# Optimization experiments

Hardware: AMD Instinct MI355X
Metric: run time of the kernel (lower is better)

## Reference

```python
import jax, jax.numpy as jnp
import numpy as np

B, T, DE, DD, A, FN, FS = 32, 2000, 512, 1024, 128, 32, 16
TEMPERATURE = 1.0


def setup_inputs() -> dict:
    key = jax.random.key(0)
    ks = jax.random.split(key, 10)
    input_enc = jax.random.normal(ks[0], (B, T, DE), dtype=jnp.float32)
    # lengths in [T//2, T] so no zero-length utterances
    enc_lengths = jax.random.randint(ks[1], (B,), T // 2, T + 1, dtype=jnp.int32)
    input_dec = jax.random.normal(ks[2], (B, DD), dtype=jnp.float32)
    # prev_att: previous-step attention weights (masked, normalized)
    prev_att = jax.random.uniform(ks[3], (B, T), dtype=jnp.float32)
    pad = jnp.arange(T)[None, :] >= enc_lengths[:, None]
    prev_att = jnp.where(pad, 0.0, prev_att)
    prev_att = prev_att / jnp.sum(prev_att, axis=1, keepdims=True)
    # parameters
    conv_w = jax.random.normal(ks[4], (FN, 1, 2 * FS + 1), dtype=jnp.float32) * 0.1  # [out,in,k]
    enc_w = jax.random.normal(ks[5], (A, DE), dtype=jnp.float32) * 0.04
    dec_w = jax.random.normal(ks[6], (A, DD), dtype=jnp.float32) * 0.03
    att_w = jax.random.normal(ks[7], (A, FN), dtype=jnp.float32) * 0.17
    att_b = jnp.zeros((A,), dtype=jnp.float32)
    out_w = jax.random.normal(ks[8], (1, A), dtype=jnp.float32) * 0.09
    return dict(input_enc=input_enc, enc_lengths=enc_lengths, input_dec=input_dec,
                prev_att=prev_att, conv_w=conv_w, enc_w=enc_w, dec_w=dec_w,
                att_w=att_w, att_b=att_b, out_w=out_w)


def reference(input_enc, enc_lengths, input_dec, prev_att,
              conv_w, enc_w, dec_w, att_w, att_b, out_w):
    b, t, _ = input_enc.shape
    fs = (conv_w.shape[-1] - 1) // 2  # 'same' padding
    # padding mask: True at padded positions t >= length
    mask = jnp.arange(t)[None, :] >= enc_lengths[:, None]  # [B,T]
    # location features: Conv1d over prev attention, 1 -> FN channels, same length
    conv = jax.lax.conv_general_dilated(
        prev_att[:, None, :], conv_w, window_strides=(1,),
        padding=[(fs, fs)], dimension_numbers=("NCH", "OIH", "NCH"))  # [B,FN,T]
    loc_feat = conv.transpose(0, 2, 1)  # [B,T,FN]
    projected_att = loc_feat @ att_w.T + att_b        # [B,T,A]
    projected_enc = input_enc @ enc_w.T               # [B,T,A]
    projected_dec = (input_dec @ dec_w.T)[:, None, :]  # [B,1,A]
    score = jnp.squeeze(jnp.tanh(projected_att + projected_enc + projected_dec) @ out_w.T, -1)  # [B,T]
    score = jnp.where(mask, -jnp.inf, score)
    att_weight = jax.nn.softmax(TEMPERATURE * score, axis=1)  # [B,T]
    context = jnp.einsum("btd,bt->bd", input_enc, att_weight)  # [B,DE]
    return context, att_weight
```

## Files before the change

### kernel.cpp

```cpp
#include <hip/hip_runtime.h>
#include <hip/hip_bf16.h>
#include <math.h>

#define B_ 32
#define T_ 2000
#define DE_ 512
#define DD_ 1024
#define A_ 128
#define FN_ 32
#define FS_ 16
#define KW_ (2*FS_+1)

typedef __bf16 bf16x8 __attribute__((ext_vector_type(8)));
typedef __bf16 bf16x4 __attribute__((ext_vector_type(4)));
typedef float f32x4 __attribute__((ext_vector_type(4)));

#define BT 64

__device__ __forceinline__ void load_lds16(const void* g, void* l) {
    __builtin_amdgcn_global_load_lds(
        (const __attribute__((address_space(1))) unsigned int*)g,
        (__attribute__((address_space(3))) unsigned int*)l, 16, 0, 0);
}

__global__ __launch_bounds__(256) void prep_kernel(
    const float* __restrict__ enc_w, const float* __restrict__ att_w,
    const float* __restrict__ input_dec, const float* __restrict__ dec_w,
    const float* __restrict__ att_b,
    __bf16* __restrict__ enc_bf, __bf16* __restrict__ att_bf,
    float* __restrict__ pdec, float* __restrict__ ctx_un )
{
    int bx = blockIdx.x, tid = threadIdx.x;
    if (bx < 64) {
        int i = bx * 256 + tid;
        float4 v = ((const float4*)enc_w)[i];
        bf16x4 o;
        o[0] = (__bf16)v.x; o[1] = (__bf16)v.y; o[2] = (__bf16)v.z; o[3] = (__bf16)v.w;
        *(bf16x4*)(enc_bf + (size_t)i * 4) = o;
        if (i < (A_ * FN_) / 4) {
            float4 w = ((const float4*)att_w)[i];
            bf16x4 p;
            p[0] = (__bf16)w.x; p[1] = (__bf16)w.y; p[2] = (__bf16)w.z; p[3] = (__bf16)w.w;
            *(bf16x4*)(att_bf + (size_t)i * 4) = p;
        }
    } else if (bx < 192) {
        int pb = bx - 64;
        int b  = pb >> 2;
        int a0 = (pb & 3) * 32;
        int al = tid >> 3;
        int kg = tid & 7;
        int a  = a0 + al;
        const float4* w = (const float4*)(dec_w + (size_t)a * DD_);
        const float4* x = (const float4*)(input_dec + (size_t)b * DD_);
        float acc = 0.f;
        #pragma unroll 8
        for (int j = 0; j < 32; j++) {
            int i4 = kg + j * 8;
            float4 wv = w[i4], xv = x[i4];
            acc += wv.x * xv.x + wv.y * xv.y + wv.z * xv.z + wv.w * xv.w;
        }
        acc += __shfl_xor(acc, 1, 64);
        acc += __shfl_xor(acc, 2, 64);
        acc += __shfl_xor(acc, 4, 64);
        if (kg == 0) pdec[b * A_ + a] = acc + att_b[a];
    } else {
        int idx = (bx - 192) * 256 + tid;
        if (idx < (B_ * DE_ + B_) / 4 + 1)
            ((float4*)ctx_un)[idx] = make_float4(0.f, 0.f, 0.f, 0.f);
    }
}

__global__ __launch_bounds__(256, 4) void score_kernel(
    const float* __restrict__ input_enc, const __bf16* __restrict__ enc_bf,
    const float* __restrict__ prev_att,  const float* __restrict__ conv_w,
    const __bf16* __restrict__ att_bf,   const float* __restrict__ pdec,
    const float* __restrict__ out_w,     const int* __restrict__ lengths,
    float* __restrict__ wbuf, float* __restrict__ ctx_un,
    float* __restrict__ denom)
{
    __shared__ __align__(16) char Bt[16384];
    __shared__ __align__(16) float cw_s[KW_ * FN_];
    __shared__ float pa_s[BT + 2 * FS_];
    __shared__ __align__(16) float w_s[BT];

    const int tid = threadIdx.x;
    const int b  = blockIdx.y;
    const int t0 = blockIdx.x * BT;
    const int len = lengths[b];

    if (t0 >= len) {
        int t = t0 + tid;
        if (tid < BT && t < T_) wbuf[b * T_ + t] = 0.f;
        return;
    }

    const int lane = tid & 63;
    const int wv   = tid >> 6;
    const int col  = lane & 15;
    const int grp  = lane >> 4;
    const int rowb = wv * 16 + col;
    const int t_row = t0 + rowb;
    const int t_clamp = t_row < T_ ? t_row : T_ - 1;
    const float* arow = input_enc + ((size_t)(b * T_ + t_clamp)) * DE_ + grp * 8;

    #pragma unroll
    for (int j = 0; j < 2; j++) {
        int s  = j * 256 + tid;
        int r  = s >> 2;
        int c  = (s & 3) ^ (r & 3);
        load_lds16(enc_bf + (size_t)r * DE_ + c * 8,
                   Bt + j * 4096 + wv * 1024);
    }
    float4 p0 = *(const float4*)(arow);
    float4 p1 = *(const float4*)(arow + 4);

    for (int j = tid; j < BT + 2 * FS_; j += 256) {
        int t = t0 - FS_ + j;
        pa_s[j] = (t >= 0 && t < T_) ? prev_att[b * T_ + t] : 0.f;
    }
    for (int idx = tid; idx < FN_ * KW_; idx += 256) {
        int f = idx / KW_, k = idx % KW_;
        cw_s[k * FN_ + f] = conv_w[idx];
    }
    __syncthreads();

    float cf[8] = {0.f,0.f,0.f,0.f,0.f,0.f,0.f,0.f};
    #pragma unroll
    for (int k = 0; k < KW_; k++) {
        float pa = pa_s[rowb + k];
        float4 c0 = *(const float4*)(cw_s + k * FN_ + grp * 8);
        float4 c1 = *(const float4*)(cw_s + k * FN_ + grp * 8 + 4);
        cf[0] += pa * c0.x; cf[1] += pa * c0.y; cf[2] += pa * c0.z; cf[3] += pa * c0.w;
        cf[4] += pa * c1.x; cf[5] += pa * c1.y; cf[6] += pa * c1.z; cf[7] += pa * c1.w;
    }

    f32x4 acc[8];
    const f32x4 zero = (f32x4){0.f, 0.f, 0.f, 0.f};

    {
        bf16x8 afrag;
        #pragma unroll
        for (int j = 0; j < 8; j++) afrag[j] = (__bf16)cf[j];
        #pragma unroll
        for (int i = 0; i < 8; i++) {
            bf16x8 bfrag = *(const bf16x8*)(att_bf + (size_t)(i * 16 + col) * FN_ + grp * 8);
            acc[i] = __builtin_amdgcn_mfma_f32_16x16x32_bf16(afrag, bfrag, zero, 0, 0, 0);
        }
    }

    const int dsoff = (grp ^ (col & 3)) * 16;

    #pragma unroll
    for (int k = 0; k < 16; k++) {
        __syncthreads();
        float4 n0, n1;
        if (k < 15) {
            int kc_next = (k + 1) * 32;
            char* half = Bt + (((k + 1) & 1) << 13);
            #pragma unroll
            for (int j = 0; j < 2; j++) {
                int s  = j * 256 + tid;
                int r  = s >> 2;
                int c  = (s & 3) ^ (r & 3);
                load_lds16(enc_bf + (size_t)r * DE_ + kc_next + c * 8,
                           half + j * 4096 + wv * 1024);
            }
            n0 = *(const float4*)(arow + kc_next);
            n1 = *(const float4*)(arow + kc_next + 4);
        }
        bf16x8 af;
        af[0] = (__bf16)p0.x; af[1] = (__bf16)p0.y;
        af[2] = (__bf16)p0.z; af[3] = (__bf16)p0.w;
        af[4] = (__bf16)p1.x; af[5] = (__bf16)p1.y;
        af[6] = (__bf16)p1.z; af[7] = (__bf16)p1.w;
        const char* half = Bt + ((k & 1) << 13);
        #pragma unroll
        for (int i = 0; i < 8; i++) {
            bf16x8 bfrag = *(const bf16x8*)(half + (i * 16 + col) * 64 + dsoff);
            acc[i] = __builtin_amdgcn_mfma_f32_16x16x32_bf16(af, bfrag, acc[i], 0, 0, 0);
        }
        p0 = n0; p1 = n1;
    }

    float s[4] = {0.f, 0.f, 0.f, 0.f};
    float Mabs = 0.f;
    #pragma unroll
    for (int i = 0; i < 8; i++) {
        int a = i * 16 + col;
        float ow = out_w[a];
        Mabs += fabsf(ow);
        float bias = pdec[b * A_ + a];
        #pragma unroll
        for (int r = 0; r < 4; r++) {
            float v = acc[i][r] + bias;
            v = fminf(fmaxf(v, -15.f), 15.f);
            float e = __expf(2.f * v);
            s[r] += ow * ((e - 1.f) / (e + 1.f));
        }
    }
    #pragma unroll
    for (int r = 0; r < 4; r++) {
        s[r] += __shfl_xor(s[r], 1, 64);
        s[r] += __shfl_xor(s[r], 2, 64);
        s[r] += __shfl_xor(s[r], 4, 64);
        s[r] += __shfl_xor(s[r], 8, 64);
    }
    Mabs += __shfl_xor(Mabs, 1, 64);
    Mabs += __shfl_xor(Mabs, 2, 64);
    Mabs += __shfl_xor(Mabs, 4, 64);
    Mabs += __shfl_xor(Mabs, 8, 64);

    if (col == 0) {
        int tb = wv * 16 + grp * 4;
        float4 wvec;
        float* wp = &wvec.x;
        #pragma unroll
        for (int r = 0; r < 4; r++) {
            int t = t0 + tb + r;
            wp[r] = (t < len) ? __expf(s[r] - Mabs) : 0.f;
        }
        *(float4*)(w_s + tb) = wvec;
        if (t0 + tb < T_) *(float4*)(wbuf + b * T_ + t0 + tb) = wvec;
    }
    __syncthreads();

    if (tid < 64) {
        float w = w_s[tid];
        w += __shfl_xor(w, 1, 64);
        w += __shfl_xor(w, 2, 64);
        w += __shfl_xor(w, 4, 64);
        w += __shfl_xor(w, 8, 64);
        w += __shfl_xor(w, 16, 64);
        w += __shfl_xor(w, 32, 64);
        if (tid == 0) atomicAdd(&denom[b], w);
    }

    int n_eff = len - t0;
    if (n_eff > BT) n_eff = BT;
    {
        int tg = tid >> 7;
        int d0 = (tid & 127) * 4;
        const float* ebase = input_enc + ((size_t)(b * T_ + t0)) * DE_ + d0;
        float cx = 0.f, cy = 0.f, cz = 0.f, cw = 0.f;
        #pragma unroll 4
        for (int t = tg; t < n_eff; t += 2) {
            float w = w_s[t];
            float4 v = *(const float4*)(ebase + (size_t)t * DE_);
            cx += w * v.x; cy += w * v.y; cz += w * v.z; cw += w * v.w;
        }
        atomicAdd(&ctx_un[b * DE_ + d0 + 0], cx);
        atomicAdd(&ctx_un[b * DE_ + d0 + 1], cy);
        atomicAdd(&ctx_un[b * DE_ + d0 + 2], cz);
        atomicAdd(&ctx_un[b * DE_ + d0 + 3], cw);
    }
}

__global__ __launch_bounds__(256) void finalize_kernel(
    const float* __restrict__ wbuf, const float* __restrict__ ctx_un,
    const float* __restrict__ denom, float* __restrict__ out)
{
    int bx = blockIdx.x, tid = threadIdx.x;
    if (bx < 64) {
        int i4 = bx * 256 + tid;
        if (i4 < (B_ * T_) / 4) {
            int b = i4 / (T_ / 4);
            float inv = 1.f / denom[b];
            float4 w = ((const float4*)wbuf)[i4];
            w.x *= inv; w.y *= inv; w.z *= inv; w.w *= inv;
            ((float4*)(out + B_ * DE_))[i4] = w;
        }
    } else {
        int j = (bx - 64) * 256 + tid;
        int b = j / (DE_ / 4);
        float inv = 1.f / denom[b];
        float4 c = ((const float4*)ctx_un)[j];
        c.x *= inv; c.y *= inv; c.z *= inv; c.w *= inv;
        ((float4*)out)[j] = c;
    }
}

extern "C" void kernel_launch(void* const* d_in, const int* in_sizes, int n_in,
                              void* d_out, int out_size, void* d_ws, size_t ws_size,
                              hipStream_t stream)
{
    const float* input_enc   = (const float*)d_in[0];
    const int*   enc_lengths = (const int*)d_in[1];
    const float* input_dec   = (const float*)d_in[2];
    const float* prev_att    = (const float*)d_in[3];
    const float* conv_w      = (const float*)d_in[4];
    const float* enc_w       = (const float*)d_in[5];
    const float* dec_w       = (const float*)d_in[6];
    const float* att_w       = (const float*)d_in[7];
    const float* att_b       = (const float*)d_in[8];
    const float* out_w       = (const float*)d_in[9];

    float* out = (float*)d_out;
    char* ws = (char*)d_ws;
    float*  pdec   = (float*)ws;
    float*  wbuf   = (float*)(ws + 16384);
    __bf16* enc_bf = (__bf16*)(ws + 272384);
    __bf16* att_bf = (__bf16*)(ws + 403456);
    float*  ctx_un = (float*)(ws + 411648);
    float*  denom  = (float*)(ws + 477184);

    prep_kernel<<<209, 256, 0, stream>>>(enc_w, att_w, input_dec, dec_w, att_b,
                                         enc_bf, att_bf, pdec, ctx_un);

    dim3 sgrid((T_ + BT - 1) / BT, B_);
    score_kernel<<<sgrid, 256, 0, stream>>>(input_enc, enc_bf, prev_att, conv_w,
                                            att_bf, pdec, out_w, enc_lengths,
                                            wbuf, ctx_un, denom);

    finalize_kernel<<<80, 256, 0, stream>>>(wbuf, ctx_un, denom, out);
}
```

Baseline: 227.3 us.

## Double score kernel time tile to 128 rows with two accumulator sets per wave

```diff
diff --git a/kernel.cpp b/kernel.cpp
--- a/kernel.cpp
+++ b/kernel.cpp
@@ -15,7 +15,7 @@
 typedef __bf16 bf16x4 __attribute__((ext_vector_type(4)));
 typedef float f32x4 __attribute__((ext_vector_type(4)));
 
-#define BT 64
+#define BT 128
 
 __device__ __forceinline__ void load_lds16(const void* g, void* l) {
     __builtin_amdgcn_global_load_lds(
@@ -70,7 +70,7 @@
     }
 }
 
-__global__ __launch_bounds__(256, 4) void score_kernel(
+__global__ __launch_bounds__(256, 2) void score_kernel(
     const float* __restrict__ input_enc, const __bf16* __restrict__ enc_bf,
     const float* __restrict__ prev_att,  const float* __restrict__ conv_w,
     const __bf16* __restrict__ att_bf,   const float* __restrict__ pdec,
@@ -78,7 +78,7 @@
     float* __restrict__ wbuf, float* __restrict__ ctx_un,
     float* __restrict__ denom)
 {
-    __shared__ __align__(16) char Bt[16384];
+    __shared__ __align__(16) char Bt[32768];
     __shared__ __align__(16) float cw_s[KW_ * FN_];
     __shared__ float pa_s[BT + 2 * FS_];
     __shared__ __align__(16) float w_s[BT];
@@ -89,8 +89,10 @@
     const int len = lengths[b];
 
     if (t0 >= len) {
-        int t = t0 + tid;
-        if (tid < BT && t < T_) wbuf[b * T_ + t] = 0.f;
+        if (tid < BT) {
+            int t = t0 + tid;
+            if (t < T_) wbuf[b * T_ + t] = 0.f;
+        }
         return;
     }
 
@@ -99,20 +101,30 @@
     const int col  = lane & 15;
     const int grp  = lane >> 4;
     const int rowb = wv * 16 + col;
-    const int t_row = t0 + rowb;
-    const int t_clamp = t_row < T_ ? t_row : T_ - 1;
-    const float* arow = input_enc + ((size_t)(b * T_ + t_clamp)) * DE_ + grp * 8;
+    const int tc0 = (t0 + rowb) < T_ ? (t0 + rowb) : T_ - 1;
+    const int tc1 = (t0 + rowb + 64) < T_ ? (t0 + rowb + 64) : T_ - 1;
+    const float* arow0 = input_enc + ((size_t)(b * T_ + tc0)) * DE_ + grp * 8;
+    const float* arow1 = input_enc + ((size_t)(b * T_ + tc1)) * DE_ + grp * 8;
 
     #pragma unroll
     for (int j = 0; j < 2; j++) {
-        int s  = j * 256 + tid;
-        int r  = s >> 2;
-        int c  = (s & 3) ^ (r & 3);
-        load_lds16(enc_bf + (size_t)r * DE_ + c * 8,
-                   Bt + j * 4096 + wv * 1024);
-    }
-    float4 p0 = *(const float4*)(arow);
-    float4 p1 = *(const float4*)(arow + 4);
+        #pragma unroll
+        for (int m = 0; m < 2; m++) {
+            int s = m * 256 + tid;
+            int r = s >> 2;
+            int c = (s & 3) ^ (r & 3);
+            load_lds16(enc_bf + (size_t)r * DE_ + j * 32 + c * 8,
+                       Bt + j * 8192 + m * 4096 + wv * 1024);
+        }
+    }
+    float4 a0p[4], a1p[4];
+    #pragma unroll
+    for (int j = 0; j < 2; j++) {
+        a0p[2*j]   = *(const float4*)(arow0 + j * 32);
+        a0p[2*j+1] = *(const float4*)(arow0 + j * 32 + 4);
+        a1p[2*j]   = *(const float4*)(arow1 + j * 32);
+        a1p[2*j+1] = *(const float4*)(arow1 + j * 32 + 4);
+    }
 
     for (int j = tid; j < BT + 2 * FS_; j += 256) {
         int t = t0 - FS_ + j;
@@ -124,65 +136,86 @@
     }
     __syncthreads();
 
-    float cf[8] = {0.f,0.f,0.f,0.f,0.f,0.f,0.f,0.f};
+    float cf0[8] = {0,0,0,0,0,0,0,0}, cf1[8] = {0,0,0,0,0,0,0,0};
     #pragma unroll
     for (int k = 0; k < KW_; k++) {
-        float pa = pa_s[rowb + k];
+        float paA = pa_s[rowb + k];
+        float paB = pa_s[rowb + 64 + k];
         float4 c0 = *(const float4*)(cw_s + k * FN_ + grp * 8);
         float4 c1 = *(const float4*)(cw_s + k * FN_ + grp * 8 + 4);
-        cf[0] += pa * c0.x; cf[1] += pa * c0.y; cf[2] += pa * c0.z; cf[3] += pa * c0.w;
-        cf[4] += pa * c1.x; cf[5] += pa * c1.y; cf[6] += pa * c1.z; cf[7] += pa * c1.w;
-    }
-
-    f32x4 acc[8];
+        cf0[0] += paA * c0.x; cf0[1] += paA * c0.y; cf0[2] += paA * c0.z; cf0[3] += paA * c0.w;
+        cf0[4] += paA * c1.x; cf0[5] += paA * c1.y; cf0[6] += paA * c1.z; cf0[7] += paA * c1.w;
+        cf1[0] += paB * c0.x; cf1[1] += paB * c0.y; cf1[2] += paB * c0.z; cf1[3] += paB * c0.w;
+        cf1[4] += paB * c1.x; cf1[5] += paB * c1.y; cf1[6] += paB * c1.z; cf1[7] += paB * c1.w;
+    }
+
+    f32x4 acc0[8], acc1[8];
     const f32x4 zero = (f32x4){0.f, 0.f, 0.f, 0.f};
 
     {
-        bf16x8 afrag;
-        #pragma unroll
-        for (int j = 0; j < 8; j++) afrag[j] = (__bf16)cf[j];
+        bf16x8 af0, af1;
+        #pragma unroll
+        for (int j = 0; j < 8; j++) { af0[j] = (__bf16)cf0[j]; af1[j] = (__bf16)cf1[j]; }
         #pragma unroll
         for (int i = 0; i < 8; i++) {
             bf16x8 bfrag = *(const bf16x8*)(att_bf + (size_t)(i * 16 + col) * FN_ + grp * 8);
-            acc[i] = __builtin_amdgcn_mfma_f32_16x16x32_bf16(afrag, bfrag, zero, 0, 0, 0);
+            acc0[i] = __builtin_amdgcn_mfma_f32_16x16x32_bf16(af0, bfrag, zero, 0, 0, 0);
+            acc1[i] = __builtin_amdgcn_mfma_f32_16x16x32_bf16(af1, bfrag, zero, 0, 0, 0);
         }
     }
 
     const int dsoff = (grp ^ (col & 3)) * 16;
 
     #pragma unroll
-    for (int k = 0; k < 16; k++) {
+    for (int k = 0; k < 8; k++) {
         __syncthreads();
-        float4 n0, n1;
-        if (k < 15) {
-            int kc_next = (k + 1) * 32;
-            char* half = Bt + (((k + 1) & 1) << 13);
+        float4 n0[4], n1[4];
+        if (k < 7) {
+            int kc_next = (k + 1) * 64;
+            char* buf = Bt + (((k + 1) & 1) << 14);
             #pragma unroll
             for (int j = 0; j < 2; j++) {
-                int s  = j * 256 + tid;
-                int r  = s >> 2;
-                int c  = (s & 3) ^ (r & 3);
-                load_lds16(enc_bf + (size_t)r * DE_ + kc_next + c * 8,
-                           half + j * 4096 + wv * 1024);
+                #pragma unroll
+                for (int m = 0; m < 2; m++) {
+                    int s = m * 256 + tid;
+                    int r = s >> 2;
+                    int c = (s & 3) ^ (r & 3);
+                    load_lds16(enc_bf + (size_t)r * DE_ + kc_next + j * 32 + c * 8,
+                               buf + j * 8192 + m * 4096 + wv * 1024);
+                }
             }
-            n0 = *(const float4*)(arow + kc_next);
-            n1 = *(const float4*)(arow + kc_next + 4);
-        }
-        bf16x8 af;
-        af[0] = (__bf16)p0.x; af[1] = (__bf16)p0.y;
-        af[2] = (__bf16)p0.z; af[3] = (__bf16)p0.w;
-        af[4] = (__bf16)p1.x; af[5] = (__bf16)p1.y;
-        af[6] = (__bf16)p1.z; af[7] = (__bf16)p1.w;
-        const char* half = Bt + ((k & 1) << 13);
-        #pragma unroll
-        for (int i = 0; i < 8; i++) {
-            bf16x8 bfrag = *(const bf16x8*)(half + (i * 16 + col) * 64 + dsoff);
-            acc[i] = __builtin_amdgcn_mfma_f32_16x16x32_bf16(af, bfrag, acc[i], 0, 0, 0);
-        }
-        p0 = n0; p1 = n1;
-    }
-
-    float s[4] = {0.f, 0.f, 0.f, 0.f};
+            #pragma unroll
+            for (int j = 0; j < 2; j++) {
+                n0[2*j]   = *(const float4*)(arow0 + kc_next + j * 32);
+                n0[2*j+1] = *(const float4*)(arow0 + kc_next + j * 32 + 4);
+                n1[2*j]   = *(const float4*)(arow1 + kc_next + j * 32);
+                n1[2*j+1] = *(const float4*)(arow1 + kc_next + j * 32 + 4);
+            }
+        }
+        const char* buf = Bt + ((k & 1) << 14);
+        #pragma unroll
+        for (int j = 0; j < 2; j++) {
+            bf16x8 af0, af1;
+            float* p;
+            p = &a0p[2*j].x;
+            #pragma unroll
+            for (int q = 0; q < 8; q++) af0[q] = (__bf16)p[q];
+            p = &a1p[2*j].x;
+            #pragma unroll
+            for (int q = 0; q < 8; q++) af1[q] = (__bf16)p[q];
+            const char* sub = buf + j * 8192;
+            #pragma unroll
+            for (int i = 0; i < 8; i++) {
+                bf16x8 bfrag = *(const bf16x8*)(sub + (i * 16 + col) * 64 + dsoff);
+                acc0[i] = __builtin_amdgcn_mfma_f32_16x16x32_bf16(af0, bfrag, acc0[i], 0, 0, 0);
+                acc1[i] = __builtin_amdgcn_mfma_f32_16x16x32_bf16(af1, bfrag, acc1[i], 0, 0, 0);
+            }
+        }
+        #pragma unroll
+        for (int q = 0; q < 4; q++) { a0p[q] = n0[q]; a1p[q] = n1[q]; }
+    }
+
+    float s0[4] = {0,0,0,0}, s1[4] = {0,0,0,0};
     float Mabs = 0.f;
     #pragma unroll
     for (int i = 0; i < 8; i++) {
@@ -192,18 +225,23 @@
         float bias = pdec[b * A_ + a];
         #pragma unroll
         for (int r = 0; r < 4; r++) {
-            float v = acc[i][r] + bias;
-            v = fminf(fmaxf(v, -15.f), 15.f);
-            float e = __expf(2.f * v);
-            s[r] += ow * ((e - 1.f) / (e + 1.f));
+            float v0 = acc0[i][r] + bias;
+            v0 = fminf(fmaxf(v0, -15.f), 15.f);
+            float e0 = __expf(2.f * v0);
+            s0[r] += ow * ((e0 - 1.f) / (e0 + 1.f));
+            float v1 = acc1[i][r] + bias;
+            v1 = fminf(fmaxf(v1, -15.f), 15.f);
+            float e1 = __expf(2.f * v1);
+            s1[r] += ow * ((e1 - 1.f) / (e1 + 1.f));
         }
     }
     #pragma unroll
     for (int r = 0; r < 4; r++) {
-        s[r] += __shfl_xor(s[r], 1, 64);
-        s[r] += __shfl_xor(s[r], 2, 64);
-        s[r] += __shfl_xor(s[r], 4, 64);
-        s[r] += __shfl_xor(s[r], 8, 64);
+        #pragma unroll
+        for (int off = 1; off < 16; off <<= 1) {
+            s0[r] += __shfl_xor(s0[r], off, 64);
+            s1[r] += __shfl_xor(s1[r], off, 64);
+        }
     }
     Mabs += __shfl_xor(Mabs, 1, 64);
     Mabs += __shfl_xor(Mabs, 2, 64);
@@ -212,26 +250,26 @@
 
     if (col == 0) {
         int tb = wv * 16 + grp * 4;
-        float4 wvec;
-        float* wp = &wvec.x;
+        float4 wv0, wv1;
+        float *p0 = &wv0.x, *p1 = &wv1.x;
         #pragma unroll
         for (int r = 0; r < 4; r++) {
-            int t = t0 + tb + r;
-            wp[r] = (t < len) ? __expf(s[r] - Mabs) : 0.f;
-        }
-        *(float4*)(w_s + tb) = wvec;
-        if (t0 + tb < T_) *(float4*)(wbuf + b * T_ + t0 + tb) = wvec;
+            int tA = t0 + tb + r;
+            int tB = tA + 64;
+            p0[r] = (tA < len) ? __expf(s0[r] - Mabs) : 0.f;
+            p1[r] = (tB < len) ? __expf(s1[r] - Mabs) : 0.f;
+        }
+        *(float4*)(w_s + tb) = wv0;
+        *(float4*)(w_s + tb + 64) = wv1;
+        if (t0 + tb < T_)      *(float4*)(wbuf + b * T_ + t0 + tb) = wv0;
+        if (t0 + tb + 64 < T_) *(float4*)(wbuf + b * T_ + t0 + tb + 64) = wv1;
     }
     __syncthreads();
 
     if (tid < 64) {
-        float w = w_s[tid];
-        w += __shfl_xor(w, 1, 64);
-        w += __shfl_xor(w, 2, 64);
-        w += __shfl_xor(w, 4, 64);
-        w += __shfl_xor(w, 8, 64);
-        w += __shfl_xor(w, 16, 64);
-        w += __shfl_xor(w, 32, 64);
+        float w = w_s[tid] + w_s[tid + 64];
+        #pragma unroll
+        for (int off = 1; off < 64; off <<= 1) w += __shfl_xor(w, off, 64);
         if (tid == 0) atomicAdd(&denom[b], w);
     }
 
```

Result: no change. 227.2 us (-0.0%).
